# Kernel tuning notes

Measured on AMD Instinct MI355X. Metric: run time of the kernel, lower is better.

## Reference

```python
import jax, jax.numpy as jnp
import numpy as np

LAYERS, BLOCKS = 10, 4
NL = LAYERS * BLOCKS
RC, DC, SC, OUT_C = 32, 32, 256, 256
B, T = 4, 32768


def setup_inputs() -> dict:
    key = jax.random.key(0)
    ks = jax.random.split(key, 6)
    s = 0.1  # keep tanh out of saturation
    return {
        "x": jax.random.normal(ks[0], (B, 1, T), jnp.float32),
        "W_start": jax.random.normal(ks[1], (RC, 1), jnp.float32) * s,
        "b_start": jnp.zeros((RC,), jnp.float32),
        "Wd": jax.random.normal(ks[2], (NL, DC, RC, 2), jnp.float32) * s,  # torch conv1d weight (out,in,k)
        "bd": jnp.zeros((NL, DC), jnp.float32),
        "Wr": jax.random.normal(ks[3], (NL, RC, DC), jnp.float32) * s,     # 1x1 residual convs
        "br": jnp.zeros((NL, RC), jnp.float32),
        "Ws": jax.random.normal(ks[4], (NL, SC, DC), jnp.float32) * s,     # 1x1 skip convs
        "bs": jnp.zeros((NL, SC), jnp.float32),
        "Wf": jax.random.normal(ks[5], (OUT_C, SC), jnp.float32) * s,      # final 1x1 conv
        "bf": jnp.zeros((OUT_C,), jnp.float32),
    }


def _forward(x, W_start, b_start, Wd, bd, Wr, br, Ws, bs, Wf, bf):
    # start 1x1 conv: [B,1,T] -> [B,RC,T]
    h = jnp.einsum('oi,bit->bot', W_start, x) + b_start[:, None]
    skip = jnp.zeros((x.shape[0], SC, x.shape[2]), x.dtype)
    for i in range(NL):  # fixed small layer loop (40)
        d = 2 ** (i % LAYERS)
        # causal dilated conv, kernel=2: out[t] = W[...,0]@x[t-d] + W[...,1]@x[t]
        h_shift = jnp.pad(h, ((0, 0), (0, 0), (d, 0)))[:, :, : h.shape[2]]
        z = (jnp.einsum('oi,bit->bot', Wd[i, :, :, 1], h)
             + jnp.einsum('oi,bit->bot', Wd[i, :, :, 0], h_shift)
             + bd[i][:, None])
        z = jnp.tanh(z)
        r = jnp.einsum('oi,bit->bot', Wr[i], z) + br[i][:, None]
        h = h + r  # residual connection
        skip = skip + jnp.einsum('oi,bit->bot', Ws[i], h) + bs[i][:, None]
    out = jax.nn.relu(skip)
    return jnp.einsum('oi,bit->bot', Wf, out) + bf[:, None]


def reference(x, W_start, b_start, Wd, bd, Wr, br, Ws, bs, Wf, bf):
    return _forward(x, W_start, b_start, Wd, bd, Wr, br, Ws, bs, Wf, bf)
```

## Files before the change

kernel.cpp:

```cpp
#include <hip/hip_runtime.h>
#include <hip/hip_bf16.h>

#define T_LEN 32768
#define B_N   4
#define RC    32
#define DC    32
#define SC    256
#define OUTC  256
#define NL    40
#define KTOT  (NL * RC)
#define NBT   (B_N * T_LEN)
#define SLOTB ((size_t)NBT * 32 * 2)
#define BTW   128
#define RING  24576

typedef float f32x4 __attribute__((ext_vector_type(4)));
typedef short bf16x8 __attribute__((ext_vector_type(8)));
typedef __attribute__((address_space(3))) unsigned int lds_u32;
typedef __attribute__((address_space(3))) char lds_char;
typedef __attribute__((address_space(1))) unsigned int glb_u32;

__device__ __forceinline__ unsigned short f2bf_bits(float f) {
    __hip_bfloat16 b = __float2bfloat16(f);
    unsigned short u;
    __builtin_memcpy(&u, &b, 2);
    return u;
}
__device__ __forceinline__ unsigned pack2(float a, float b) {
    return (unsigned)f2bf_bits(a) | ((unsigned)f2bf_bits(b) << 16);
}
__device__ __forceinline__ float bflo(unsigned u) { return __uint_as_float((u & 0xFFFFu) << 16); }
__device__ __forceinline__ float bfhi(unsigned u) { return __uint_as_float(u & 0xFFFF0000u); }
__device__ __forceinline__ float ftanh(float x) {
    float e = __expf(2.f * x);
    return 1.f - 2.f / (e + 1.f);
}
__device__ __forceinline__ int swz(int L) { return L ^ ((((L >> 7) & 3)) << 4); }
__device__ __forceinline__ void wait_vmcnt(int n) {
    switch (n) {
        case 0: asm volatile("s_waitcnt vmcnt(0)" ::: "memory"); break;
        case 6: asm volatile("s_waitcnt vmcnt(6)" ::: "memory"); break;
        default: asm volatile("s_waitcnt vmcnt(12)" ::: "memory"); break;
    }
}

__global__ __launch_bounds__(256) void k_prep(const float* __restrict__ Ws,
                                              const float* __restrict__ Wf,
                                              const float* __restrict__ Wd,
                                              const float* __restrict__ Wr,
                                              const float* __restrict__ bs,
                                              unsigned short* __restrict__ Wsk2,
                                              unsigned short* __restrict__ Wfk,
                                              unsigned short* __restrict__ Wd1k,
                                              unsigned short* __restrict__ Wd0k,
                                              unsigned short* __restrict__ Wrk,
                                              float* __restrict__ bs_sum) {
    int g = blockIdx.x * 256 + threadIdx.x;
    if (g < SC * KTOT) {
        int i = g >> 13, r = g & 8191;
        int oc = r >> 5, c = r & 31;
        Wsk2[g] = f2bf_bits(Ws[(i * SC + oc) * RC + c]);
        return;
    }
    g -= SC * KTOT;
    if (g < OUTC * SC) { Wfk[g] = f2bf_bits(Wf[g]); return; }
    g -= OUTC * SC;
    if (g < NL * 1024) {
        int i = g >> 10, r = g & 1023;
        int o = r >> 5, c = r & 31;
        Wd1k[g] = f2bf_bits(Wd[((i * DC + o) * RC + c) * 2 + 1]);
        return;
    }
    g -= NL * 1024;
    if (g < NL * 1024) {
        int i = g >> 10, r = g & 1023;
        int o = r >> 5, c = r & 31;
        Wd0k[g] = f2bf_bits(Wd[((i * DC + o) * RC + c) * 2 + 0]);
        return;
    }
    g -= NL * 1024;
    if (g < NL * 1024) { Wrk[g] = f2bf_bits(Wr[g]); return; }
    g -= NL * 1024;
    if (g < SC) {
        float s = 0.f;
        for (int i = 0; i < NL; ++i) s += bs[i * SC + g];
        bs_sum[g] = s;
    }
}

__global__ __launch_bounds__(256) void k_start(const float* __restrict__ x,
                                               const float* __restrict__ Wst,
                                               const float* __restrict__ bst,
                                               unsigned short* __restrict__ h0) {
    int g = blockIdx.x * 256 + threadIdx.x;
    float xv = x[g];
    unsigned u[16];
#pragma unroll
    for (int q = 0; q < 16; ++q) {
        float a = Wst[2 * q] * xv + bst[2 * q];
        float b = Wst[2 * q + 1] * xv + bst[2 * q + 1];
        u[q] = pack2(a, b);
    }
    unsigned short* op = h0 + (size_t)g * 32;
#pragma unroll
    for (int q = 0; q < 4; ++q) *(uint4*)&op[q * 8] = *(uint4*)&u[q * 4];
}

__global__ __launch_bounds__(256, 4) void k_layer(const unsigned short* __restrict__ hprev,
                                                  unsigned short* __restrict__ hnext,
                                                  const unsigned short* __restrict__ Wd1k,
                                                  const unsigned short* __restrict__ Wd0k,
                                                  const unsigned short* __restrict__ Wrk,
                                                  const float* __restrict__ bd,
                                                  const float* __restrict__ br,
                                                  int d) {
    __shared__ unsigned short zbuf[4][32 * 40];
    int lane = threadIdx.x & 63;
    int wq = threadIdx.x >> 6;
    int lr = lane & 15, lg = lane >> 4;
    int btb = blockIdx.x * 128 + wq * 32;
    unsigned short* zp = &zbuf[wq][0];

    bf16x8 wd1[2], wd0[2], wr[2];
#pragma unroll
    for (int m = 0; m < 2; ++m) {
        int ao = (m * 16 + lr) * 32 + 8 * lg;
        wd1[m] = *(const bf16x8*)(Wd1k + ao);
        wd0[m] = *(const bf16x8*)(Wd0k + ao);
        wr[m]  = *(const bf16x8*)(Wrk + ao);
    }

    bf16x8 hc[2], hs[2];
    uint2 hcc[2][2];
#pragma unroll
    for (int n = 0; n < 2; ++n) {
        int bt = btb + n * 16 + lr;
        int t = bt & (T_LEN - 1);
        const unsigned short* hp = hprev + (size_t)bt * 32;
        hc[n] = *(const bf16x8*)(hp + 8 * lg);
        int bts = (t >= d) ? (bt - d) : bt;
        bf16x8 v = *(const bf16x8*)(hprev + (size_t)bts * 32 + 8 * lg);
        if (t < d) v = (bf16x8){0, 0, 0, 0, 0, 0, 0, 0};
        hs[n] = v;
#pragma unroll
        for (int m = 0; m < 2; ++m) hcc[n][m] = *(const uint2*)(hp + m * 16 + 4 * lg);
    }

    f32x4 zac[2][2];
#pragma unroll
    for (int m = 0; m < 2; ++m)
#pragma unroll
        for (int n = 0; n < 2; ++n) {
            f32x4 a = __builtin_amdgcn_mfma_f32_16x16x32_bf16(wd0[m], hs[n], (f32x4){0.f, 0.f, 0.f, 0.f}, 0, 0, 0);
            zac[m][n] = __builtin_amdgcn_mfma_f32_16x16x32_bf16(wd1[m], hc[n], a, 0, 0, 0);
        }

#pragma unroll
    for (int m = 0; m < 2; ++m) {
        float4 bdv = *(const float4*)(bd + m * 16 + 4 * lg);
#pragma unroll
        for (int n = 0; n < 2; ++n) {
            int rbt = n * 16 + lr;
            float z0 = ftanh(zac[m][n][0] + bdv.x);
            float z1 = ftanh(zac[m][n][1] + bdv.y);
            float z2 = ftanh(zac[m][n][2] + bdv.z);
            float z3 = ftanh(zac[m][n][3] + bdv.w);
            uint2 u;
            u.x = pack2(z0, z1);
            u.y = pack2(z2, z3);
            *(uint2*)(zp + rbt * 40 + m * 16 + 4 * lg) = u;
        }
    }

    f32x4 racc[2][2];
#pragma unroll
    for (int n = 0; n < 2; ++n) {
        int rbt = n * 16 + lr;
        bf16x8 zb = *(const bf16x8*)(zp + rbt * 40 + 8 * lg);
#pragma unroll
        for (int m = 0; m < 2; ++m)
            racc[m][n] = __builtin_amdgcn_mfma_f32_16x16x32_bf16(wr[m], zb, (f32x4){0.f, 0.f, 0.f, 0.f}, 0, 0, 0);
    }

#pragma unroll
    for (int m = 0; m < 2; ++m) {
        float4 brv = *(const float4*)(br + m * 16 + 4 * lg);
#pragma unroll
        for (int n = 0; n < 2; ++n) {
            int bt = btb + n * 16 + lr;
            float h0 = bflo(hcc[n][m].x) + racc[m][n][0] + brv.x;
            float h1 = bfhi(hcc[n][m].x) + racc[m][n][1] + brv.y;
            float h2 = bflo(hcc[n][m].y) + racc[m][n][2] + brv.z;
            float h3 = bfhi(hcc[n][m].y) + racc[m][n][3] + brv.w;
            uint2 u;
            u.x = pack2(h0, h1);
            u.y = pack2(h2, h3);
            *(uint2*)(hnext + (size_t)bt * 32 + m * 16 + 4 * lg) = u;
        }
    }
}

__global__ __launch_bounds__(256, 2) void k_skipfinal(const unsigned short* __restrict__ hist,
                                                      const unsigned short* __restrict__ Wsk2,
                                                      const unsigned short* __restrict__ Wfk,
                                                      const float* __restrict__ bs_sum,
                                                      const float* __restrict__ bfv,
                                                      float* __restrict__ outp) {
    __shared__ char smem[73728];
    const int tid = threadIdx.x;
    const int lane = tid & 63, wq = tid >> 6;
    const int lr = lane & 15, lg = lane >> 4;
    const int wm = wq & 1, wn = wq >> 1;
    const int bt0 = blockIdx.x * BTW;
    const char* histb = (const char*)hist;
    const char* Wsb = (const char*)Wsk2;
    lds_char* smem3 = (lds_char*)smem;

    int asrc[4], bsrc[2];
#pragma unroll
    for (int p = 0; p < 4; ++p) asrc[p] = swz(p * 4096 + tid * 16);
#pragma unroll
    for (int p = 0; p < 2; ++p) bsrc[p] = bt0 * 64 + swz(p * 4096 + tid * 16);

    auto stage = [&](int k) {
        int sl = NL - 1 - k;
        char* base = smem + (k % 3) * RING;
#pragma unroll
        for (int p = 0; p < 4; ++p)
            __builtin_amdgcn_global_load_lds((const glb_u32*)(Wsb + (size_t)sl * 16384 + asrc[p]),
                                             (lds_u32*)(base + p * 4096 + tid * 16), 16, 0, 0);
#pragma unroll
        for (int p = 0; p < 2; ++p)
            __builtin_amdgcn_global_load_lds((const glb_u32*)(histb + (size_t)sl * SLOTB + bsrc[p]),
                                             (lds_u32*)(base + 16384 + p * 4096 + tid * 16), 16, 0, 0);
    };

    f32x4 acc[8][4];
#pragma unroll
    for (int m = 0; m < 8; ++m)
#pragma unroll
        for (int n = 0; n < 4; ++n) acc[m][n] = (f32x4){0.f, 0.f, 0.f, 0.f};

    const int cswz = (lg * 16) ^ (((lr >> 1) & 3) << 4);
    const int arow = wm * 128 + lr;
    const int brow = wn * 64 + lr;

    stage(0);
    stage(1);
    stage(2);

#pragma unroll
    for (int i = 0; i < NL; ++i) {
        if (i >= 1 && i + 2 < NL) stage(i + 2);
        wait_vmcnt(i + 2 < NL ? 12 : (i + 1 < NL ? 6 : 0));
        __builtin_amdgcn_s_barrier();

        lds_char* Ab = smem3 + (i % 3) * RING;
        lds_char* Bb = Ab + 16384;
        bf16x8 af[8], bb[4];
#pragma unroll
        for (int m = 0; m < 8; ++m)
            asm volatile("ds_read_b128 %0, %1" : "=v"(af[m]) : "v"(Ab + (arow + m * 16) * 64 + cswz));
#pragma unroll
        for (int n = 0; n < 4; ++n)
            asm volatile("ds_read_b128 %0, %1" : "=v"(bb[n]) : "v"(Bb + (brow + n * 16) * 64 + cswz));
        asm volatile("s_waitcnt lgkmcnt(0)" ::: "memory");
        __builtin_amdgcn_sched_barrier(0);

#pragma unroll
        for (int m = 0; m < 8; ++m)
#pragma unroll
            for (int n = 0; n < 4; ++n)
                acc[m][n] = __builtin_amdgcn_mfma_f32_16x16x32_bf16(af[m], bb[n], acc[m][n], 0, 0, 0);
        __builtin_amdgcn_s_barrier();
    }
    __syncthreads();

    char* skb = smem;
#pragma unroll
    for (int m = 0; m < 8; ++m) {
        int oc0 = wm * 128 + m * 16 + lg * 4;
        float c0 = bs_sum[oc0], c1 = bs_sum[oc0 + 1], c2 = bs_sum[oc0 + 2], c3 = bs_sum[oc0 + 3];
#pragma unroll
        for (int n = 0; n < 4; ++n) {
            int bt = wn * 64 + n * 16 + lr;
            f32x4 v = acc[m][n];
            uint2 u;
            u.x = pack2(fmaxf(v[0] + c0, 0.f), fmaxf(v[1] + c1, 0.f));
            u.y = pack2(fmaxf(v[2] + c2, 0.f), fmaxf(v[3] + c3, 0.f));
            int L = bt * 512 + oc0 * 2;
            *(uint2*)(skb + (L ^ ((bt & 7) << 4))) = u;
        }
    }
    __syncthreads();

#pragma unroll
    for (int m = 0; m < 8; ++m)
#pragma unroll
        for (int n = 0; n < 4; ++n) acc[m][n] = (f32x4){0.f, 0.f, 0.f, 0.f};

    const unsigned short* Fb = Wfk + (size_t)(wm * 128 + lr) * SC + 8 * lg;

#pragma unroll
    for (int kk = 0; kk < SC / 32; ++kk) {
        bf16x8 fa[8];
#pragma unroll
        for (int m = 0; m < 8; ++m) fa[m] = *(const bf16x8*)(Fb + (size_t)m * 16 * SC + kk * 32);
        bf16x8 sbv[4];
#pragma unroll
        for (int n = 0; n < 4; ++n) {
            int bt = wn * 64 + n * 16 + lr;
            int L = bt * 512 + kk * 64 + lg * 16;
            sbv[n] = *(const bf16x8*)(skb + (L ^ ((bt & 7) << 4)));
        }
#pragma unroll
        for (int m = 0; m < 8; ++m)
#pragma unroll
            for (int n = 0; n < 4; ++n)
                acc[m][n] = __builtin_amdgcn_mfma_f32_16x16x32_bf16(fa[m], sbv[n], acc[m][n], 0, 0, 0);
    }

    int b2 = bt0 >> 15;
    int t0 = bt0 & (T_LEN - 1);
#pragma unroll
    for (int m = 0; m < 8; ++m) {
        int o0 = wm * 128 + m * 16 + lg * 4;
        float q0 = bfv[o0], q1 = bfv[o0 + 1], q2 = bfv[o0 + 2], q3 = bfv[o0 + 3];
#pragma unroll
        for (int n = 0; n < 4; ++n) {
            int t = t0 + wn * 64 + n * 16 + lr;
            f32x4 v = acc[m][n];
            outp[((size_t)(b2 * OUTC + o0 + 0) << 15) + t] = v[0] + q0;
            outp[((size_t)(b2 * OUTC + o0 + 1) << 15) + t] = v[1] + q1;
            outp[((size_t)(b2 * OUTC + o0 + 2) << 15) + t] = v[2] + q2;
            outp[((size_t)(b2 * OUTC + o0 + 3) << 15) + t] = v[3] + q3;
        }
    }
}

extern "C" void kernel_launch(void* const* d_in, const int* in_sizes, int n_in,
                              void* d_out, int out_size, void* d_ws, size_t ws_size,
                              hipStream_t stream) {
    const float* x       = (const float*)d_in[0];
    const float* W_start = (const float*)d_in[1];
    const float* b_start = (const float*)d_in[2];
    const float* Wd      = (const float*)d_in[3];
    const float* bd      = (const float*)d_in[4];
    const float* Wr      = (const float*)d_in[5];
    const float* br      = (const float*)d_in[6];
    const float* Ws      = (const float*)d_in[7];
    const float* bs      = (const float*)d_in[8];
    const float* Wf      = (const float*)d_in[9];
    const float* bfv     = (const float*)d_in[10];

    char* wsb = (char*)d_ws;
    unsigned short* Wsk2 = (unsigned short*)(wsb);
    unsigned short* Wfk  = (unsigned short*)(wsb + 655360);
    unsigned short* Wd1k = (unsigned short*)(wsb + 786432);
    unsigned short* Wd0k = (unsigned short*)(wsb + 868352);
    unsigned short* Wrk  = (unsigned short*)(wsb + 950272);
    float*          bs_sum = (float*)(wsb + 1032192);
    char* S1 = wsb + (1 << 20);
    char* X  = S1 + 40 * SLOTB;

    auto slotptr = [&](int i) -> unsigned short* {
        return (unsigned short*)(i == 0 ? X : S1 + (size_t)(i - 1) * SLOTB);
    };

    k_prep<<<(SC * KTOT + OUTC * SC + 3 * NL * 1024 + SC + 255) / 256, 256, 0, stream>>>(
        Ws, Wf, Wd, Wr, bs, Wsk2, Wfk, Wd1k, Wd0k, Wrk, bs_sum);
    k_start<<<NBT / 256, 256, 0, stream>>>(x, W_start, b_start, slotptr(0));

    for (int i = 0; i < NL; ++i) {
        int d = 1 << (i % 10);
        k_layer<<<NBT / 128, 256, 0, stream>>>(slotptr(i), slotptr(i + 1),
                                               Wd1k + i * 1024, Wd0k + i * 1024, Wrk + i * 1024,
                                               bd + i * DC, br + i * RC, d);
    }

    k_skipfinal<<<NBT / BTW, 256, 0, stream>>>((unsigned short*)S1, Wsk2, Wfk, bs_sum, bfv, (float*)d_out);
}
```

Baseline: 420.1 us.

## Fuse pairs of low-dilation layers into one kernel with LDS halo

Adds k_layer2, which computes two consecutive dilated layers per block. The intermediate h is kept in swizzled LDS with a 128-step halo recomputed from the previous slot, and is still written out for the skip pass. For dilations 1 to 128 the launches are paired, cutting the layer kernel count from 40 to 24 and removing the global re-read of the intermediate activation for the second layer. The cost is redundant halo computation, 512-thread blocks and more LDS per block, which may lower occupancy.

```diff
diff --git a/kernel.cpp b/kernel.cpp
--- a/kernel.cpp
+++ b/kernel.cpp
@@ -13,6 +13,7 @@
 #define SLOTB ((size_t)NBT * 32 * 2)
 #define BTW   128
 #define RING  24576
+#define H2    128
 
 typedef float f32x4 __attribute__((ext_vector_type(4)));
 typedef short bf16x8 __attribute__((ext_vector_type(8)));
@@ -36,6 +37,7 @@
     return 1.f - 2.f / (e + 1.f);
 }
 __device__ __forceinline__ int swz(int L) { return L ^ ((((L >> 7) & 3)) << 4); }
+__device__ __forceinline__ int midaddr(int u, int c) { return u * 64 + (c ^ (((u >> 1) & 3) << 4)); }
 __device__ __forceinline__ void wait_vmcnt(int n) {
     switch (n) {
         case 0: asm volatile("s_waitcnt vmcnt(0)" ::: "memory"); break;
@@ -200,6 +202,180 @@
     }
 }
 
+__global__ __launch_bounds__(512, 2) void k_layer2(const unsigned short* __restrict__ hin,
+                                                   unsigned short* __restrict__ hmid,
+                                                   unsigned short* __restrict__ hfin,
+                                                   const unsigned short* __restrict__ W1a,
+                                                   const unsigned short* __restrict__ W0a,
+                                                   const unsigned short* __restrict__ Wra,
+                                                   const float* __restrict__ bda,
+                                                   const float* __restrict__ bra,
+                                                   const unsigned short* __restrict__ W1b,
+                                                   const unsigned short* __restrict__ W0b,
+                                                   const unsigned short* __restrict__ Wrb,
+                                                   const float* __restrict__ bdb,
+                                                   const float* __restrict__ brb,
+                                                   int d1, int d2) {
+    __shared__ char midb[384 * 64];
+    __shared__ unsigned short zbuf[8][32 * 40];
+    const int tid = threadIdx.x;
+    const int lane = tid & 63, wq = tid >> 6;
+    const int lr = lane & 15, lg = lane >> 4;
+    const int bt0 = blockIdx.x * 256;
+    unsigned short* zp = &zbuf[wq][0];
+
+    bf16x8 wd1[2], wd0[2], wr[2];
+    float4 bdv[2], brv[2];
+#pragma unroll
+    for (int m = 0; m < 2; ++m) {
+        int ao = (m * 16 + lr) * 32 + 8 * lg;
+        wd1[m] = *(const bf16x8*)(W1a + ao);
+        wd0[m] = *(const bf16x8*)(W0a + ao);
+        wr[m]  = *(const bf16x8*)(Wra + ao);
+        bdv[m] = *(const float4*)(bda + m * 16 + 4 * lg);
+        brv[m] = *(const float4*)(bra + m * 16 + 4 * lg);
+    }
+
+#pragma unroll 1
+    for (int pass = 0; pass < 2; ++pass) {
+        int tl = (pass == 0) ? wq : (wq + 8);
+        if (pass == 1 && wq >= 4) break;
+        int btb = bt0 - H2 + tl * 32;
+
+        bf16x8 hc[2], hs[2];
+        uint2 hcc[2][2];
+#pragma unroll
+        for (int n = 0; n < 2; ++n) {
+            int bt = btb + n * 16 + lr;
+            int btc = bt < 0 ? 0 : bt;
+            int t = btc & (T_LEN - 1);
+            const unsigned short* hp = hin + (size_t)btc * 32;
+            hc[n] = *(const bf16x8*)(hp + 8 * lg);
+            int bts = (t >= d1) ? (btc - d1) : btc;
+            bf16x8 v = *(const bf16x8*)(hin + (size_t)bts * 32 + 8 * lg);
+            if (t < d1) v = (bf16x8){0, 0, 0, 0, 0, 0, 0, 0};
+            hs[n] = v;
+#pragma unroll
+            for (int m = 0; m < 2; ++m) hcc[n][m] = *(const uint2*)(hp + m * 16 + 4 * lg);
+        }
+
+        f32x4 zac[2][2];
+#pragma unroll
+        for (int m = 0; m < 2; ++m)
+#pragma unroll
+            for (int n = 0; n < 2; ++n) {
+                f32x4 a = __builtin_amdgcn_mfma_f32_16x16x32_bf16(wd0[m], hs[n], (f32x4){0.f, 0.f, 0.f, 0.f}, 0, 0, 0);
+                zac[m][n] = __builtin_amdgcn_mfma_f32_16x16x32_bf16(wd1[m], hc[n], a, 0, 0, 0);
+            }
+#pragma unroll
+        for (int m = 0; m < 2; ++m)
+#pragma unroll
+            for (int n = 0; n < 2; ++n) {
+                int rbt = n * 16 + lr;
+                uint2 u;
+                u.x = pack2(ftanh(zac[m][n][0] + bdv[m].x), ftanh(zac[m][n][1] + bdv[m].y));
+                u.y = pack2(ftanh(zac[m][n][2] + bdv[m].z), ftanh(zac[m][n][3] + bdv[m].w));
+                *(uint2*)(zp + rbt * 40 + m * 16 + 4 * lg) = u;
+            }
+        f32x4 racc[2][2];
+#pragma unroll
+        for (int n = 0; n < 2; ++n) {
+            bf16x8 zb = *(const bf16x8*)(zp + (n * 16 + lr) * 40 + 8 * lg);
+#pragma unroll
+            for (int m = 0; m < 2; ++m)
+                racc[m][n] = __builtin_amdgcn_mfma_f32_16x16x32_bf16(wr[m], zb, (f32x4){0.f, 0.f, 0.f, 0.f}, 0, 0, 0);
+        }
+#pragma unroll
+        for (int m = 0; m < 2; ++m)
+#pragma unroll
+            for (int n = 0; n < 2; ++n) {
+                int bt = btb + n * 16 + lr;
+                int u_ = bt - (bt0 - H2);
+                float h0 = bflo(hcc[n][m].x) + racc[m][n][0] + brv[m].x;
+                float h1 = bfhi(hcc[n][m].x) + racc[m][n][1] + brv[m].y;
+                float h2 = bflo(hcc[n][m].y) + racc[m][n][2] + brv[m].z;
+                float h3 = bfhi(hcc[n][m].y) + racc[m][n][3] + brv[m].w;
+                uint2 u;
+                u.x = pack2(h0, h1);
+                u.y = pack2(h2, h3);
+                *(uint2*)(midb + midaddr(u_, m * 32 + lg * 8)) = u;
+                if (bt >= bt0)
+                    *(uint2*)(hmid + (size_t)bt * 32 + m * 16 + 4 * lg) = u;
+            }
+    }
+    __syncthreads();
+
+#pragma unroll
+    for (int m = 0; m < 2; ++m) {
+        int ao = (m * 16 + lr) * 32 + 8 * lg;
+        wd1[m] = *(const bf16x8*)(W1b + ao);
+        wd0[m] = *(const bf16x8*)(W0b + ao);
+        wr[m]  = *(const bf16x8*)(Wrb + ao);
+        bdv[m] = *(const float4*)(bdb + m * 16 + 4 * lg);
+        brv[m] = *(const float4*)(brb + m * 16 + 4 * lg);
+    }
+
+    {
+        int btb = bt0 + wq * 32;
+        bf16x8 hc[2], hs[2];
+        uint2 hcc[2][2];
+#pragma unroll
+        for (int n = 0; n < 2; ++n) {
+            int bt = btb + n * 16 + lr;
+            int t = bt & (T_LEN - 1);
+            int u_ = bt - (bt0 - H2);
+            hc[n] = *(const bf16x8*)(midb + midaddr(u_, lg * 16));
+            bf16x8 v = *(const bf16x8*)(midb + midaddr(u_ - d2, lg * 16));
+            if (t < d2) v = (bf16x8){0, 0, 0, 0, 0, 0, 0, 0};
+            hs[n] = v;
+#pragma unroll
+            for (int m = 0; m < 2; ++m)
+                hcc[n][m] = *(const uint2*)(midb + midaddr(u_, m * 32 + lg * 8));
+        }
+
+        f32x4 zac[2][2];
+#pragma unroll
+        for (int m = 0; m < 2; ++m)
+#pragma unroll
+            for (int n = 0; n < 2; ++n) {
+                f32x4 a = __builtin_amdgcn_mfma_f32_16x16x32_bf16(wd0[m], hs[n], (f32x4){0.f, 0.f, 0.f, 0.f}, 0, 0, 0);
+                zac[m][n] = __builtin_amdgcn_mfma_f32_16x16x32_bf16(wd1[m], hc[n], a, 0, 0, 0);
+            }
+#pragma unroll
+        for (int m = 0; m < 2; ++m)
+#pragma unroll
+            for (int n = 0; n < 2; ++n) {
+                int rbt = n * 16 + lr;
+                uint2 u;
+                u.x = pack2(ftanh(zac[m][n][0] + bdv[m].x), ftanh(zac[m][n][1] + bdv[m].y));
+                u.y = pack2(ftanh(zac[m][n][2] + bdv[m].z), ftanh(zac[m][n][3] + bdv[m].w));
+                *(uint2*)(zp + rbt * 40 + m * 16 + 4 * lg) = u;
+            }
+        f32x4 racc[2][2];
+#pragma unroll
+        for (int n = 0; n < 2; ++n) {
+            bf16x8 zb = *(const bf16x8*)(zp + (n * 16 + lr) * 40 + 8 * lg);
+#pragma unroll
+            for (int m = 0; m < 2; ++m)
+                racc[m][n] = __builtin_amdgcn_mfma_f32_16x16x32_bf16(wr[m], zb, (f32x4){0.f, 0.f, 0.f, 0.f}, 0, 0, 0);
+        }
+#pragma unroll
+        for (int m = 0; m < 2; ++m)
+#pragma unroll
+            for (int n = 0; n < 2; ++n) {
+                int bt = btb + n * 16 + lr;
+                float h0 = bflo(hcc[n][m].x) + racc[m][n][0] + brv[m].x;
+                float h1 = bfhi(hcc[n][m].x) + racc[m][n][1] + brv[m].y;
+                float h2 = bflo(hcc[n][m].y) + racc[m][n][2] + brv[m].z;
+                float h3 = bfhi(hcc[n][m].y) + racc[m][n][3] + brv[m].w;
+                uint2 u;
+                u.x = pack2(h0, h1);
+                u.y = pack2(h2, h3);
+                *(uint2*)(hfin + (size_t)bt * 32 + m * 16 + 4 * lg) = u;
+            }
+    }
+}
+
 __global__ __launch_bounds__(256, 2) void k_skipfinal(const unsigned short* __restrict__ hist,
                                                       const unsigned short* __restrict__ Wsk2,
                                                       const unsigned short* __restrict__ Wfk,
@@ -371,11 +547,23 @@
         Ws, Wf, Wd, Wr, bs, Wsk2, Wfk, Wd1k, Wd0k, Wrk, bs_sum);
     k_start<<<NBT / 256, 256, 0, stream>>>(x, W_start, b_start, slotptr(0));
 
-    for (int i = 0; i < NL; ++i) {
-        int d = 1 << (i % 10);
-        k_layer<<<NBT / 128, 256, 0, stream>>>(slotptr(i), slotptr(i + 1),
-                                               Wd1k + i * 1024, Wd0k + i * 1024, Wrk + i * 1024,
-                                               bd + i * DC, br + i * RC, d);
+    for (int g = 0; g < 4; ++g) {
+        int base = g * 10;
+        for (int j = 0; j < 8; j += 2) {
+            int i = base + j;
+            k_layer2<<<NBT / 256, 512, 0, stream>>>(
+                slotptr(i), slotptr(i + 1), slotptr(i + 2),
+                Wd1k + i * 1024, Wd0k + i * 1024, Wrk + i * 1024, bd + i * DC, br + i * RC,
+                Wd1k + (i + 1) * 1024, Wd0k + (i + 1) * 1024, Wrk + (i + 1) * 1024,
+                bd + (i + 1) * DC, br + (i + 1) * RC,
+                1 << j, 1 << (j + 1));
+        }
+        for (int j = 8; j < 10; ++j) {
+            int i = base + j;
+            k_layer<<<NBT / 128, 256, 0, stream>>>(slotptr(i), slotptr(i + 1),
+                                                   Wd1k + i * 1024, Wd0k + i * 1024, Wrk + i * 1024,
+                                                   bd + i * DC, br + i * RC, 1 << j);
+        }
     }
 
     k_skipfinal<<<NBT / BTW, 256, 0, stream>>>((unsigned short*)S1, Wsk2, Wfk, bs_sum, bfv, (float*)d_out);
```

Measured after the change: 416.1 us. About the same (-1.0%).
